# Kernel tuning notes

Measured on AMD Instinct MI355X. Metric: run time of the kernel, lower is better.

Reference implementation:

```python
import jax, jax.numpy as jnp
import numpy as np

N, IN, HID, OUT = 8192, 128, 256, 64

def setup_inputs() -> dict:
    key = jax.random.key(0)
    k = jax.random.split(key, 6)
    s1 = 1.0 / np.sqrt(IN)
    s2 = 1.0 / np.sqrt(HID)
    return {
        "x": jax.random.normal(k[0], (N, IN), dtype=jnp.float32),
        "adj": jax.random.uniform(k[1], (N, N), dtype=jnp.float32),
        "W1": jax.random.uniform(k[2], (HID, IN), jnp.float32, -s1, s1),
        "b1": jax.random.uniform(k[3], (HID,), jnp.float32, -s1, s1),
        "W2": jax.random.uniform(k[4], (OUT, HID), jnp.float32, -s2, s2),
        "b2": jax.random.uniform(k[5], (OUT,), jnp.float32, -s2, s2),
    }

def reference(x, adj, W1, b1, W2, b2):
    # deg_inv_sqrt @ adj @ deg_inv_sqrt == row/col elementwise scaling (same math,
    # without materializing diagonal matrices or doing O(N^3) GEMMs)
    deg = adj.sum(axis=1)
    d = 1.0 / jnp.sqrt(deg + 1e-8)  # [N]
    norm_adj = d[:, None] * adj * d[None, :]  # [N, N]
    h = jax.nn.relu((norm_adj @ x) @ W1.T + b1)  # [N, HID]
    return (norm_adj @ h) @ W2.T + b2  # [N, OUT]
```

## Files before the change

kernel.cpp:

```cpp
#include <hip/hip_runtime.h>
#include <hip/hip_bf16.h>

typedef float f32x4 __attribute__((ext_vector_type(4)));
typedef int   i32x4 __attribute__((ext_vector_type(4)));
typedef int   i32x2 __attribute__((ext_vector_type(2)));
typedef __bf16 bf16x8 __attribute__((ext_vector_type(8)));
typedef __bf16 bf16x4 __attribute__((ext_vector_type(4)));

#define N_NODES 8192
#define IN_F    128
#define HID_F   256
#define OUT_F   64
#define SPLIT1  8
#define SPLIT2  16

__device__ __forceinline__ void dma16(const void* g, void* l) {
  __builtin_amdgcn_global_load_lds(
      (const __attribute__((address_space(1))) void*)g,
      (__attribute__((address_space(3))) void*)(uint32_t)(uintptr_t)l, 16, 0, 0);
}

template <int K> __device__ __forceinline__ void wait_vmcnt() {
  if constexpr (K == 0)       asm volatile("s_waitcnt vmcnt(0)" ::: "memory");
  else if constexpr (K == 4)  asm volatile("s_waitcnt vmcnt(4)" ::: "memory");
  else if constexpr (K == 5)  asm volatile("s_waitcnt vmcnt(5)" ::: "memory");
  else if constexpr (K == 8)  asm volatile("s_waitcnt vmcnt(8)" ::: "memory");
  else if constexpr (K == 10) asm volatile("s_waitcnt vmcnt(10)" ::: "memory");
  else if constexpr (K == 12) asm volatile("s_waitcnt vmcnt(12)" ::: "memory");
  else if constexpr (K == 15) asm volatile("s_waitcnt vmcnt(15)" ::: "memory");
  else static_assert(K == 0, "unsupported vmcnt literal");
}

__global__ __launch_bounds__(256) void k_degcvt(const float* __restrict__ adj,
                                                char* __restrict__ adjq,
                                                float* __restrict__ d) {
  const int row = blockIdx.x;
  const int t = threadIdx.x;
  const f32x4* p = (const f32x4*)(adj + (size_t)row * N_NODES);
  i32x2* qo = (i32x2*)(adjq + (size_t)row * N_NODES);
  float s = 0.f;
#pragma unroll
  for (int i = 0; i < N_NODES / (256 * 8); ++i) {
    f32x4 a = p[i * 512 + 2 * t];
    f32x4 b = p[i * 512 + 2 * t + 1];
    s += a[0] + a[1] + a[2] + a[3] + b[0] + b[1] + b[2] + b[3];
    int q0 = __float2int_rn(fmaf(a[0], 254.f, -127.f));
    int q1 = __float2int_rn(fmaf(a[1], 254.f, -127.f));
    int q2 = __float2int_rn(fmaf(a[2], 254.f, -127.f));
    int q3 = __float2int_rn(fmaf(a[3], 254.f, -127.f));
    int q4 = __float2int_rn(fmaf(b[0], 254.f, -127.f));
    int q5 = __float2int_rn(fmaf(b[1], 254.f, -127.f));
    int q6 = __float2int_rn(fmaf(b[2], 254.f, -127.f));
    int q7 = __float2int_rn(fmaf(b[3], 254.f, -127.f));
    i32x2 o;
    o[0] = (q0 & 255) | ((q1 & 255) << 8) | ((q2 & 255) << 16) | ((q3 & 255) << 24);
    o[1] = (q4 & 255) | ((q5 & 255) << 8) | ((q6 & 255) << 16) | ((q7 & 255) << 24);
    qo[i * 256 + t] = o;
  }
#pragma unroll
  for (int off = 32; off > 0; off >>= 1) s += __shfl_down(s, off);
  __shared__ float red[4];
  if ((t & 63) == 0) red[t >> 6] = s;
  __syncthreads();
  if (t == 0) d[row] = rsqrtf(red[0] + red[1] + red[2] + red[3] + 1e-8f);
}

__global__ __launch_bounds__(256) void k_bt1q(const float* __restrict__ x,
                                              const float* __restrict__ d,
                                              char* __restrict__ Q1,
                                              float* __restrict__ s1v,
                                              float* __restrict__ csv) {
  __shared__ float col[N_NODES];
  __shared__ float redmx[4];
  __shared__ int psI[4][SPLIT1];
  const int c = blockIdx.x, t = threadIdx.x;
  const int w = t >> 6;
  float mx = 0.f;
#pragma unroll
  for (int i = 0; i < 8; ++i) {
    const int j0 = i * 1024 + t * 4;
#pragma unroll
    for (int k = 0; k < 4; ++k) {
      float v = x[(size_t)(j0 + k) * IN_F + c] * d[j0 + k];
      col[j0 + k] = v;
      mx = fmaxf(mx, fabsf(v));
    }
  }
#pragma unroll
  for (int off = 32; off > 0; off >>= 1) mx = fmaxf(mx, __shfl_down(mx, off));
  if ((t & 63) == 0) redmx[t >> 6] = mx;
  __syncthreads();
  mx = fmaxf(fmaxf(redmx[0], redmx[1]), fmaxf(redmx[2], redmx[3]));
  mx = fmaxf(mx, 1e-20f);
  const float s1 = mx * (1.f / 127.f);
  const float r1 = 127.f / mx;
  if (t == 0) s1v[c] = s1;
  int qsum[SPLIT1];
#pragma unroll
  for (int i = 0; i < 8; ++i) {
    const int j0 = i * 1024 + t * 4;
    int w1 = 0, qs = 0;
#pragma unroll
    for (int k = 0; k < 4; ++k) {
      int q1 = __float2int_rn(col[j0 + k] * r1);
      w1 |= (q1 & 255) << (8 * k);
      qs += q1;
    }
    *(int*)(Q1 + (size_t)c * N_NODES + j0) = w1;
    qsum[i] = qs;
  }
#pragma unroll
  for (int i = 0; i < SPLIT1; ++i)
#pragma unroll
    for (int off = 32; off > 0; off >>= 1) qsum[i] += __shfl_down(qsum[i], off);
  if ((t & 63) == 0) {
#pragma unroll
    for (int i = 0; i < SPLIT1; ++i) psI[w][i] = qsum[i];
  }
  __syncthreads();
  if (t < SPLIT1)
    csv[t * IN_F + c] =
        s1 * (float)(psI[0][t] + psI[1][t] + psI[2][t] + psI[3][t]);
}

__device__ inline bf16x8 load_frag(const float* p) {
  f32x4 a = *(const f32x4*)p;
  f32x4 b = *(const f32x4*)(p + 4);
  bf16x8 o = {(__bf16)a[0], (__bf16)a[1], (__bf16)a[2], (__bf16)a[3],
              (__bf16)b[0], (__bf16)b[1], (__bf16)b[2], (__bf16)b[3]};
  return o;
}

template <int WGM, int WGN, int KC, int KWAIT>
__device__ __forceinline__ void g_iter(char* sm, int it, int w,
                                       const char* (&a_src)[WGM],
                                       const char* (&b_src)[WGN],
                                       const int (&offA)[4],
                                       const int (&offB)[4],
                                       i32x4 (&acc)[4][4]) {
  constexpr int BM = WGM * 64, BN = WGN * 64;
  constexpr int ABYTES = BM * 64;
  constexpr int STAGE = (BM + BN) * 64;
  constexpr int NIT = KC / 64;

  if (it + 3 < NIT) {
    char* nb = sm + ((it + 3) & 3) * STAGE;
#pragma unroll
    for (int kk = 0; kk < WGM; ++kk) {
      dma16(a_src[kk], nb + kk * 4096 + (w << 10));
      a_src[kk] += 64;
    }
#pragma unroll
    for (int kk = 0; kk < WGN; ++kk) {
      dma16(b_src[kk], nb + ABYTES + kk * 4096 + (w << 10));
      b_src[kk] += 64;
    }
  }
  __builtin_amdgcn_sched_barrier(0);
  wait_vmcnt<KWAIT>();
  asm volatile("s_barrier" ::: "memory");
  __builtin_amdgcn_sched_barrier(0);

  const char* cb = sm + (it & 3) * STAGE;
  i32x4 af[4], bf[4];
#pragma unroll
  for (int tm = 0; tm < 4; ++tm) af[tm] = *(const i32x4*)(cb + offA[tm]);
#pragma unroll
  for (int ct = 0; ct < 4; ++ct) bf[ct] = *(const i32x4*)(cb + offB[ct]);
#pragma unroll
  for (int tm = 0; tm < 4; ++tm)
#pragma unroll
    for (int ct = 0; ct < 4; ++ct)
      acc[tm][ct] = __builtin_amdgcn_mfma_i32_16x16x64_i8(af[tm], bf[ct],
                                                          acc[tm][ct], 0, 0, 0);
  __builtin_amdgcn_sched_barrier(0);
  asm volatile("s_waitcnt lgkmcnt(0)" ::: "memory");
  asm volatile("s_barrier" ::: "memory");
}

template <int WGM, int WGN, int KC>
__global__ __launch_bounds__(256, 2) void k_gemm_i8(
    const char* __restrict__ A, const char* __restrict__ B,
    const float* __restrict__ s1v, const float* __restrict__ csq,
    __bf16* __restrict__ P) {
  constexpr int BM = WGM * 64, BN = WGN * 64;
  constexpr int ANI = WGM, BNI = WGN;
  constexpr int ABYTES = BM * 64;
  constexpr int STAGE = (BM + BN) * 64;
  constexpr int NIT = KC / 64;
  constexpr int L = ANI + BNI;
  static_assert(NIT > 3, "pipeline needs >3 K-steps");

  __shared__ __align__(16) char sm[4 * STAGE];

  const int t = threadIdx.x;
  const int w = t >> 6, lane = t & 63;
  const int r = lane & 15, q = lane >> 4;
  const int wm = (WGN == 1) ? w : (w >> 1);
  const int wn = (WGN == 1) ? 0 : (w & 1);
  const int m0 = blockIdx.x * BM;
  const int ks = blockIdx.y;
  const int k0 = ks * KC;

  const int n_ = t >> 2;
  const int csw = (t & 3) ^ ((t >> 3) & 3);
  const char* a_src[ANI];
  const char* b_src[BNI];
#pragma unroll
  for (int kk = 0; kk < ANI; ++kk)
    a_src[kk] = A + (size_t)(m0 + n_ + 64 * kk) * N_NODES + k0 + csw * 16;
#pragma unroll
  for (int kk = 0; kk < BNI; ++kk)
    b_src[kk] = B + (size_t)(n_ + 64 * kk) * N_NODES + k0 + csw * 16;

  int offA[4], offB[4];
#pragma unroll
  for (int tm = 0; tm < 4; ++tm) {
    const int row = wm * 64 + tm * 16 + r;
    offA[tm] = row * 64 + ((q ^ ((row >> 1) & 3)) << 4);
  }
#pragma unroll
  for (int ct = 0; ct < 4; ++ct) {
    const int row = wn * 64 + ct * 16 + r;
    offB[ct] = ABYTES + row * 64 + ((q ^ ((row >> 1) & 3)) << 4);
  }

  i32x4 acc[4][4];
#pragma unroll
  for (int tm = 0; tm < 4; ++tm)
#pragma unroll
    for (int ct = 0; ct < 4; ++ct) acc[tm][ct] = (i32x4){0, 0, 0, 0};

#pragma unroll
  for (int s = 0; s < 3; ++s) {
    char* sb = sm + s * STAGE;
#pragma unroll
    for (int kk = 0; kk < ANI; ++kk) {
      dma16(a_src[kk], sb + kk * 4096 + (w << 10));
      a_src[kk] += 64;
    }
#pragma unroll
    for (int kk = 0; kk < BNI; ++kk) {
      dma16(b_src[kk], sb + ABYTES + kk * 4096 + (w << 10));
      b_src[kk] += 64;
    }
  }

  for (int it = 0; it < NIT - 3; ++it)
    g_iter<WGM, WGN, KC, 3 * L>(sm, it, w, a_src, b_src, offA, offB, acc);
  g_iter<WGM, WGN, KC, 2 * L>(sm, NIT - 3, w, a_src, b_src, offA, offB, acc);
  g_iter<WGM, WGN, KC, L>(sm, NIT - 2, w, a_src, b_src, offA, offB, acc);
  g_iter<WGM, WGN, KC, 0>(sm, NIT - 1, w, a_src, b_src, offA, offB, acc);

  __bf16* pout =
      P + ((size_t)ks * N_NODES + m0 + wm * 64 + q * 4) * BN + wn * 64 + r;
#pragma unroll
  for (int ct = 0; ct < 4; ++ct) {
    const int col = wn * 64 + ct * 16 + r;
    const float s1c = s1v[col];
    const float corr = 127.f * csq[ks * BN + col];
#pragma unroll
    for (int tm = 0; tm < 4; ++tm)
#pragma unroll
      for (int i = 0; i < 4; ++i)
        pout[(size_t)(tm * 16 + i) * BN + ct * 16] =
            (__bf16)((s1c * (float)acc[tm][ct][i] + corr) * (1.f / 254.f));
  }
}

__global__ __launch_bounds__(256) void k_red_mlp(const __bf16* __restrict__ P1,
                                                 const float* __restrict__ dvec,
                                                 const float* __restrict__ W1,
                                                 const float* __restrict__ b1,
                                                 const float* __restrict__ W2,
                                                 float* __restrict__ Gf) {
  __shared__ __align__(16) float y[16][IN_F + 4];
  __shared__ __align__(16) __bf16 h[16][HID_F + 8];
  __shared__ __align__(16) float gl[OUT_F][20];
  __shared__ float dl[16];
  const int t = threadIdx.x;
  const int lane = t & 63;
  const int w = t >> 6;
  const int r = lane & 15, q = lane >> 4;
  const int j0 = blockIdx.x * 16;

  if (t < 16) dl[t] = dvec[j0 + t];
  const size_t planeB4 = (size_t)N_NODES * IN_F / 4;
  for (int e = t; e < 16 * IN_F / 4; e += 256) {
    const int jj = e >> 5, c4 = e & 31;
    const size_t base = (size_t)(j0 + jj) * (IN_F / 4) + c4;
    f32x4 v = (f32x4){0.f, 0.f, 0.f, 0.f};
#pragma unroll
    for (int s = 0; s < SPLIT1; ++s) {
      bf16x4 b = ((const bf16x4*)P1)[base + s * planeB4];
      v[0] += (float)b[0]; v[1] += (float)b[1];
      v[2] += (float)b[2]; v[3] += (float)b[3];
    }
    const float dj = dvec[j0 + jj];
    v *= dj;
    *(f32x4*)&y[jj][c4 * 4] = v;
  }
  __syncthreads();

  f32x4 hacc[4];
#pragma unroll
  for (int tt = 0; tt < 4; ++tt) hacc[tt] = (f32x4){0.f, 0.f, 0.f, 0.f};
#pragma unroll
  for (int kt = 0; kt < 4; ++kt) {
    bf16x8 afr = load_frag((const float*)&y[r][kt * 32 + q * 8]);
#pragma unroll
    for (int tt = 0; tt < 4; ++tt) {
      const int col = w * 64 + tt * 16 + r;
      bf16x8 bfr = load_frag(W1 + (size_t)col * IN_F + kt * 32 + q * 8);
      hacc[tt] = __builtin_amdgcn_mfma_f32_16x16x32_bf16(afr, bfr, hacc[tt], 0, 0, 0);
    }
  }
#pragma unroll
  for (int tt = 0; tt < 4; ++tt) {
    const int col = w * 64 + tt * 16 + r;
    const float bias = b1[col];
#pragma unroll
    for (int i = 0; i < 4; ++i)
      h[q * 4 + i][col] = (__bf16)fmaxf(hacc[tt][i] + bias, 0.f);
  }
  __syncthreads();

  f32x4 gacc = (f32x4){0.f, 0.f, 0.f, 0.f};
  const int o = w * 16 + r;
#pragma unroll
  for (int kt = 0; kt < 8; ++kt) {
    bf16x8 afr = *(const bf16x8*)&h[r][kt * 32 + q * 8];
    bf16x8 bfr = load_frag(W2 + (size_t)o * HID_F + kt * 32 + q * 8);
    gacc = __builtin_amdgcn_mfma_f32_16x16x32_bf16(afr, bfr, gacc, 0, 0, 0);
  }
#pragma unroll
  for (int i = 0; i < 4; ++i) gl[o][q * 4 + i] = gacc[i];
  __syncthreads();

  const int oo = t >> 2, r0 = (t & 3) * 4;
  f32x4 ov;
#pragma unroll
  for (int rr = 0; rr < 4; ++rr) ov[rr] = gl[oo][r0 + rr] * dl[r0 + rr];
  *(f32x4*)(Gf + (size_t)oo * N_NODES + j0 + r0) = ov;
}

__global__ __launch_bounds__(256) void k_quant2(const float* __restrict__ G,
                                                char* __restrict__ Q1,
                                                float* __restrict__ s1v,
                                                float* __restrict__ csv) {
  __shared__ float redmx[4];
  __shared__ int psI[4][8];
  const int o = blockIdx.x, t = threadIdx.x;
  const int w = t >> 6;
  const float* row = G + (size_t)o * N_NODES;
  f32x4 vv[8];
  float mx = 0.f;
#pragma unroll
  for (int i = 0; i < 8; ++i) {
    vv[i] = ((const f32x4*)row)[i * 256 + t];
    mx = fmaxf(mx, fmaxf(fmaxf(fabsf(vv[i][0]), fabsf(vv[i][1])),
                         fmaxf(fabsf(vv[i][2]), fabsf(vv[i][3]))));
  }
#pragma unroll
  for (int off = 32; off > 0; off >>= 1) mx = fmaxf(mx, __shfl_down(mx, off));
  if ((t & 63) == 0) redmx[t >> 6] = mx;
  __syncthreads();
  mx = fmaxf(fmaxf(redmx[0], redmx[1]), fmaxf(redmx[2], redmx[3]));
  mx = fmaxf(mx, 1e-20f);
  const float s1 = mx * (1.f / 127.f);
  const float r1 = 127.f / mx;
  if (t == 0) s1v[o] = s1;
  int qc[8];
#pragma unroll
  for (int i = 0; i < 8; ++i) {
    const int j0 = i * 1024 + t * 4;
    int w1 = 0, qs = 0;
#pragma unroll
    for (int k = 0; k < 4; ++k) {
      int q1 = __float2int_rn(vv[i][k] * r1);
      w1 |= (q1 & 255) << (8 * k);
      qs += q1;
    }
    *(int*)(Q1 + (size_t)o * N_NODES + j0) = w1;
    qc[i] = qs;
  }
#pragma unroll
  for (int i = 0; i < 8; ++i)
#pragma unroll
    for (int off = 32; off > 0; off >>= 1) qc[i] += __shfl_down(qc[i], off);
  if ((t & 63) == 0) {
#pragma unroll
    for (int i = 0; i < 8; ++i) psI[w][i] = qc[i];
  }
  __syncthreads();
  if (t < SPLIT2) {
    const int i = t >> 1;
    const int sum = (t & 1) ? psI[2][i] + psI[3][i] : psI[0][i] + psI[1][i];
    csv[t * OUT_F + o] = s1 * (float)sum;
  }
}

__global__ __launch_bounds__(256) void k_out(const __bf16* __restrict__ P2,
                                             const float* __restrict__ dvec,
                                             const float* __restrict__ b2,
                                             float* __restrict__ out) {
  const int idx = blockIdx.x * 256 + threadIdx.x;
  const int j = idx >> 4, o4 = idx & 15;
  const size_t planeB4 = (size_t)N_NODES * OUT_F / 4;
  f32x4 s = (f32x4){0.f, 0.f, 0.f, 0.f};
#pragma unroll
  for (int sp = 0; sp < SPLIT2; ++sp) {
    bf16x4 b = ((const bf16x4*)P2)[idx + sp * planeB4];
    s[0] += (float)b[0]; s[1] += (float)b[1];
    s[2] += (float)b[2]; s[3] += (float)b[3];
  }
  s *= dvec[j];
  s += ((const f32x4*)b2)[o4];
  ((f32x4*)out)[idx] = s;
}

extern "C" void kernel_launch(void* const* d_in, const int* in_sizes, int n_in,
                              void* d_out, int out_size, void* d_ws,
                              size_t ws_size, hipStream_t stream) {
  const float* x   = (const float*)d_in[0];
  const float* adj = (const float*)d_in[1];
  const float* W1  = (const float*)d_in[2];
  const float* b1  = (const float*)d_in[3];
  const float* W2  = (const float*)d_in[4];
  const float* b2  = (const float*)d_in[5];
  float* out = (float*)d_out;
  char* ws = (char*)d_ws;

  size_t off = 0;
  char*  adjq  = ws + off;            off += (size_t)N_NODES * N_NODES;
  float* dvec  = (float*)(ws + off);  off += (size_t)N_NODES * 4;
  char*  Q1b1  = ws + off;            off += (size_t)IN_F * N_NODES;
  float* s1b1  = (float*)(ws + off);  off += 1024;
  float* cs1   = (float*)(ws + off);  off += (size_t)SPLIT1 * IN_F * 4 + 256;
  __bf16* P1   = (__bf16*)(ws + off); off += (size_t)SPLIT1 * N_NODES * IN_F * 2;
  float* Gf    = (float*)(ws + off);  off += (size_t)OUT_F * N_NODES * 4;
  char*  Q1b2  = ws + off;            off += (size_t)OUT_F * N_NODES;
  float* s1b2  = (float*)(ws + off);  off += 1024;
  float* cs2   = (float*)(ws + off);  off += (size_t)SPLIT2 * OUT_F * 4 + 256;
  __bf16* P2   = (__bf16*)(ws + off);

  hipLaunchKernelGGL(k_degcvt, dim3(N_NODES), dim3(256), 0, stream, adj, adjq, dvec);
  hipLaunchKernelGGL(k_bt1q, dim3(IN_F), dim3(256), 0, stream, x, dvec,
                     Q1b1, s1b1, cs1);
  hipLaunchKernelGGL((k_gemm_i8<2, 2, N_NODES / SPLIT1>),
                     dim3(N_NODES / 128, SPLIT1), dim3(256), 0, stream,
                     adjq, Q1b1, s1b1, cs1, P1);
  hipLaunchKernelGGL(k_red_mlp, dim3(N_NODES / 16), dim3(256), 0, stream, P1,
                     dvec, W1, b1, W2, Gf);
  hipLaunchKernelGGL(k_quant2, dim3(OUT_F), dim3(256), 0, stream, Gf,
                     Q1b2, s1b2, cs2);
  hipLaunchKernelGGL((k_gemm_i8<4, 1, N_NODES / SPLIT2>),
                     dim3(N_NODES / 256, SPLIT2), dim3(256), 0, stream,
                     adjq, Q1b2, s1b2, cs2, P2);
  hipLaunchKernelGGL(k_out, dim3((N_NODES * OUT_F / 4) / 256), dim3(256), 0,
                     stream, P2, dvec, b2, out);
}
```

Measured before the change: 452.6 us.

## Use single-barrier LDS ring buffer with configurable prefetch depth in int8 GEMM

Removes the trailing lgkmcnt wait and second barrier in each GEMM K-iteration by enlarging the LDS ring beyond the prefetch distance (NB >= D+2), so a stage being overwritten is never one still being read. Prefetch depth and ring size become template parameters: GEMM1 uses depth 3 with 5 buffers, GEMM2 uses depth 2 with 4 buffers. This halves the barriers per step but uses more LDS, which could limit occupancy, and GEMM2 gets a shallower prefetch.

```diff
diff --git a/kernel.cpp b/kernel.cpp
--- a/kernel.cpp
+++ b/kernel.cpp
@@ -27,7 +27,6 @@
   else if constexpr (K == 8)  asm volatile("s_waitcnt vmcnt(8)" ::: "memory");
   else if constexpr (K == 10) asm volatile("s_waitcnt vmcnt(10)" ::: "memory");
   else if constexpr (K == 12) asm volatile("s_waitcnt vmcnt(12)" ::: "memory");
-  else if constexpr (K == 15) asm volatile("s_waitcnt vmcnt(15)" ::: "memory");
   else static_assert(K == 0, "unsupported vmcnt literal");
 }
 
@@ -131,7 +130,7 @@
   return o;
 }
 
-template <int WGM, int WGN, int KC, int KWAIT>
+template <int WGM, int WGN, int KC, int D, int NB, int KWAIT>
 __device__ __forceinline__ void g_iter(char* sm, int it, int w,
                                        const char* (&a_src)[WGM],
                                        const char* (&b_src)[WGN],
@@ -143,8 +142,8 @@
   constexpr int STAGE = (BM + BN) * 64;
   constexpr int NIT = KC / 64;
 
-  if (it + 3 < NIT) {
-    char* nb = sm + ((it + 3) & 3) * STAGE;
+  if (it + D < NIT) {
+    char* nb = sm + ((it + D) % NB) * STAGE;
 #pragma unroll
     for (int kk = 0; kk < WGM; ++kk) {
       dma16(a_src[kk], nb + kk * 4096 + (w << 10));
@@ -161,7 +160,7 @@
   asm volatile("s_barrier" ::: "memory");
   __builtin_amdgcn_sched_barrier(0);
 
-  const char* cb = sm + (it & 3) * STAGE;
+  const char* cb = sm + (it % NB) * STAGE;
   i32x4 af[4], bf[4];
 #pragma unroll
   for (int tm = 0; tm < 4; ++tm) af[tm] = *(const i32x4*)(cb + offA[tm]);
@@ -173,12 +172,9 @@
     for (int ct = 0; ct < 4; ++ct)
       acc[tm][ct] = __builtin_amdgcn_mfma_i32_16x16x64_i8(af[tm], bf[ct],
                                                           acc[tm][ct], 0, 0, 0);
-  __builtin_amdgcn_sched_barrier(0);
-  asm volatile("s_waitcnt lgkmcnt(0)" ::: "memory");
-  asm volatile("s_barrier" ::: "memory");
-}
-
-template <int WGM, int WGN, int KC>
+}
+
+template <int WGM, int WGN, int KC, int D, int NB>
 __global__ __launch_bounds__(256, 2) void k_gemm_i8(
     const char* __restrict__ A, const char* __restrict__ B,
     const float* __restrict__ s1v, const float* __restrict__ csq,
@@ -189,9 +185,11 @@
   constexpr int STAGE = (BM + BN) * 64;
   constexpr int NIT = KC / 64;
   constexpr int L = ANI + BNI;
-  static_assert(NIT > 3, "pipeline needs >3 K-steps");
-
-  __shared__ __align__(16) char sm[4 * STAGE];
+  static_assert(NIT > D, "pipeline needs >D K-steps");
+  static_assert(NB >= D + 2, "single-barrier ring needs NB >= D+2");
+  static_assert(NB * STAGE <= 81920, "2 blocks/CU LDS budget");
+
+  __shared__ __align__(16) char sm[NB * STAGE];
 
   const int t = threadIdx.x;
   const int w = t >> 6, lane = t & 63;
@@ -232,7 +230,7 @@
     for (int ct = 0; ct < 4; ++ct) acc[tm][ct] = (i32x4){0, 0, 0, 0};
 
 #pragma unroll
-  for (int s = 0; s < 3; ++s) {
+  for (int s = 0; s < D; ++s) {
     char* sb = sm + s * STAGE;
 #pragma unroll
     for (int kk = 0; kk < ANI; ++kk) {
@@ -246,11 +244,16 @@
     }
   }
 
-  for (int it = 0; it < NIT - 3; ++it)
-    g_iter<WGM, WGN, KC, 3 * L>(sm, it, w, a_src, b_src, offA, offB, acc);
-  g_iter<WGM, WGN, KC, 2 * L>(sm, NIT - 3, w, a_src, b_src, offA, offB, acc);
-  g_iter<WGM, WGN, KC, L>(sm, NIT - 2, w, a_src, b_src, offA, offB, acc);
-  g_iter<WGM, WGN, KC, 0>(sm, NIT - 1, w, a_src, b_src, offA, offB, acc);
+  for (int it = 0; it < NIT - D; ++it)
+    g_iter<WGM, WGN, KC, D, NB, D * L>(sm, it, w, a_src, b_src, offA, offB, acc);
+  if constexpr (D == 3) {
+    g_iter<WGM, WGN, KC, D, NB, 2 * L>(sm, NIT - 3, w, a_src, b_src, offA, offB, acc);
+    g_iter<WGM, WGN, KC, D, NB, 1 * L>(sm, NIT - 2, w, a_src, b_src, offA, offB, acc);
+    g_iter<WGM, WGN, KC, D, NB, 0>(sm, NIT - 1, w, a_src, b_src, offA, offB, acc);
+  } else {
+    g_iter<WGM, WGN, KC, D, NB, 1 * L>(sm, NIT - 2, w, a_src, b_src, offA, offB, acc);
+    g_iter<WGM, WGN, KC, D, NB, 0>(sm, NIT - 1, w, a_src, b_src, offA, offB, acc);
+  }
 
   __bf16* pout =
       P + ((size_t)ks * N_NODES + m0 + wm * 64 + q * 4) * BN + wn * 64 + r;
@@ -447,14 +450,14 @@
   hipLaunchKernelGGL(k_degcvt, dim3(N_NODES), dim3(256), 0, stream, adj, adjq, dvec);
   hipLaunchKernelGGL(k_bt1q, dim3(IN_F), dim3(256), 0, stream, x, dvec,
                      Q1b1, s1b1, cs1);
-  hipLaunchKernelGGL((k_gemm_i8<2, 2, N_NODES / SPLIT1>),
+  hipLaunchKernelGGL((k_gemm_i8<2, 2, N_NODES / SPLIT1, 3, 5>),
                      dim3(N_NODES / 128, SPLIT1), dim3(256), 0, stream,
                      adjq, Q1b1, s1b1, cs1, P1);
   hipLaunchKernelGGL(k_red_mlp, dim3(N_NODES / 16), dim3(256), 0, stream, P1,
                      dvec, W1, b1, W2, Gf);
   hipLaunchKernelGGL(k_quant2, dim3(OUT_F), dim3(256), 0, stream, Gf,
                      Q1b2, s1b2, cs2);
-  hipLaunchKernelGGL((k_gemm_i8<4, 1, N_NODES / SPLIT2>),
+  hipLaunchKernelGGL((k_gemm_i8<4, 1, N_NODES / SPLIT2, 2, 4>),
                      dim3(N_NODES / 256, SPLIT2), dim3(256), 0, stream,
                      adjq, Q1b2, s1b2, cs2, P2);
   hipLaunchKernelGGL(k_out, dim3((N_NODES * OUT_F / 4) / 256), dim3(256), 0,
```

Measured after the change: 452.9 us. About the same (+0.1%).
